# Kernel optimization log

Hardware: AMD Instinct MI355X
Metric: run time of the kernel (lower is better)

## Reference

```python
import jax, jax.numpy as jnp
import numpy as np

N, K, D = 16384, 8192, 256  # flattened tokens, codebook size, token dim


def setup_inputs() -> dict:
    key = jax.random.key(0)
    k1, k2 = jax.random.split(key)
    inputs_flatten = jax.random.normal(k1, (N, D), dtype=jnp.float32)
    embed = jax.random.normal(k2, (K, D), dtype=jnp.float32)
    return {"inputs_flatten": inputs_flatten, "embed": embed}


def reference(inputs_flatten, embed):
    x_sq = jnp.sum(inputs_flatten ** 2, axis=1, keepdims=True)          # [N, 1]
    e_sq = jnp.sum(embed ** 2, axis=1)                                  # [K]
    distances = x_sq + e_sq - 2.0 * (inputs_flatten @ embed.T)          # [N, K]
    encoding_indices = jnp.argmin(distances, axis=1)                    # [N]
    # encodings @ embed with one-hot encodings == gather rows of embed
    quantize = embed[encoding_indices]                                  # [N, D]
    # straight-through estimator
    quantize = jax.lax.stop_gradient(quantize - inputs_flatten) + inputs_flatten
    return quantize, encoding_indices[:, None]
```

## Files before the change

### kernel.cpp

```cpp
#include <hip/hip_runtime.h>
#include <float.h>
#include <limits.h>
#include <stdint.h>

constexpr int N = 16384;
constexpr int K = 8192;
constexpr int D = 256;

typedef _Float16 half8_t __attribute__((ext_vector_type(8)));
typedef float float4_t __attribute__((ext_vector_type(4)));

__global__ void vq_rowsq(const float* __restrict__ A, float* __restrict__ out) {
    int row = blockIdx.x;
    int lane = threadIdx.x;
    float4 v = ((const float4*)(A + (size_t)row * D))[lane];
    float s = v.x * v.x + v.y * v.y + v.z * v.z + v.w * v.w;
    #pragma unroll
    for (int o = 32; o > 0; o >>= 1) s += __shfl_down(s, o);
    if (lane == 0) out[row] = s;
}


__global__ void vq_prep(const float* __restrict__ X, const float* __restrict__ E,
                        _Float16* __restrict__ Xh, _Float16* __restrict__ Eh,
                        float* __restrict__ esq) {
    int c = blockIdx.x * 256 + threadIdx.x;
    const int XCH = N * 32;
    if (c < XCH) {
        int row = c >> 5, q8 = c & 31;
        int ds = q8 >> 2, q = q8 & 3;
        int rt = row >> 7, lr = row & 127;
        int slot = ((lr >> 4) << 6) + (q << 4) + (lr & 15);
        size_t dst = ((size_t)rt * 4096 + ds * 512 + slot) * 8;
        const float4* s4 = (const float4*)(X + (size_t)row * D + q8 * 8);
        float4 v0 = s4[0], v1 = s4[1];
        float x[8] = {v0.x, v0.y, v0.z, v0.w, v1.x, v1.y, v1.z, v1.w};
        half8_t hh;
        #pragma unroll
        for (int i = 0; i < 8; i++) hh[i] = (_Float16)x[i];
        *(half8_t*)(Xh + dst) = hh;
    } else {
        int cc = c - XCH;
        int code = cc >> 5, q8 = cc & 31;
        int ds = q8 >> 2, q = q8 & 3;
        int ct = code >> 7, lc = code & 127;
        int slot = ((lc >> 4) << 6) + (q << 4) + (lc & 15);
        size_t dst = ((size_t)(ct * 8 + ds) * 512 + slot) * 8;
        const float4* s4 = (const float4*)(E + (size_t)code * D + q8 * 8);
        float4 v0 = s4[0], v1 = s4[1];
        float x[8] = {v0.x, v0.y, v0.z, v0.w, v1.x, v1.y, v1.z, v1.w};
        half8_t hh;
        float sq = 0.f;
        #pragma unroll
        for (int i = 0; i < 8; i++) {
            hh[i] = (_Float16)x[i];
            sq += x[i] * x[i];
        }
        *(half8_t*)(Eh + dst) = hh;
        #pragma unroll
        for (int o = 16; o > 0; o >>= 1) sq += __shfl_xor(sq, o);
        if ((threadIdx.x & 31) == 0) esq[code] = sq;
    }
}

__device__ __forceinline__ void ldg_lds16(const _Float16* g, _Float16* l) {
    __builtin_amdgcn_global_load_lds(
        (const __attribute__((address_space(1))) unsigned int*)g,
        (__attribute__((address_space(3))) unsigned int*)l, 16, 0, 0);
}

constexpr int CS = 8;
constexpr int KT = (K / 128) / CS;
constexpr int NSTEP = KT * 8;

__global__ __launch_bounds__(256, 2) void vq_mfma(
    const _Float16* __restrict__ Xh, const _Float16* __restrict__ Eh,
    const float* __restrict__ esq, float4* __restrict__ pcand) {
    __shared__ _Float16 lds[32768];

    const int t = threadIdx.x, w = t >> 6, lane = t & 63;
    const int rt = blockIdx.x;
    const int cs = blockIdx.y;
    const int c15 = lane & 15, quad = lane >> 4;

    float best[16];
    int bidx[16];
    #pragma unroll
    for (int i = 0; i < 16; i++) { best[i] = FLT_MAX; bidx[i] = 0; }

    {
        const _Float16* src = Xh + ((size_t)rt * 4096 + w * 1024) * 8;
        _Float16* dst = lds + (size_t)(w * 1024) * 8;
        #pragma unroll
        for (int i = 0; i < 16; i++)
            ldg_lds16(src + (size_t)(i * 64 + lane) * 8, dst + i * 512);
    }

    const half8_t* C = (const half8_t*)lds;
    const int abase = (w >> 1) * 256 + lane;
    const half8_t* Bf = (const half8_t*)Eh;
    const int bbase = (w & 1) * 256 + lane;

    float4_t acc[4][4];
    #pragma unroll
    for (int mt = 0; mt < 4; mt++)
        #pragma unroll
        for (int nt = 0; nt < 4; nt++) acc[mt][nt] = {0.f, 0.f, 0.f, 0.f};

    half8_t Breg[2][4];
    auto loadB = [&](int s, int par) {
        const size_t rbase = (size_t)(cs * KT * 8 + s) * 512 + bbase;
        #pragma unroll
        for (int nt = 0; nt < 4; nt++) Breg[par][nt] = Bf[rbase + nt * 64];
    };

    loadB(0, 0);
    __syncthreads();

    #pragma unroll 2
    for (int s = 0; s < NSTEP; s++) {
        if (s + 1 < NSTEP) loadB(s + 1, (s + 1) & 1);

        const int ds = s & 7;
        half8_t A[4];
        #pragma unroll
        for (int mt = 0; mt < 4; mt++) A[mt] = C[ds * 512 + abase + mt * 64];

        #pragma unroll
        for (int mt = 0; mt < 4; mt++)
            #pragma unroll
            for (int nt = 0; nt < 4; nt++)
                acc[mt][nt] = __builtin_amdgcn_mfma_f32_16x16x32_f16(
                    A[mt], Breg[s & 1][nt], acc[mt][nt], 0, 0, 0);

        if ((s & 7) == 7) {
            const int code0 = (cs * KT + (s >> 3)) * 128 + (w & 1) * 64;
            #pragma unroll
            for (int nt = 0; nt < 4; nt++) {
                const int code = code0 + nt * 16 + c15;
                const float eq = esq[code];
                #pragma unroll
                for (int mt = 0; mt < 4; mt++)
                    #pragma unroll
                    for (int rg = 0; rg < 4; rg++) {
                        float sc = fmaf(-2.f, acc[mt][nt][rg], eq);
                        int sl = mt * 4 + rg;
                        if (sc < best[sl]) { best[sl] = sc; bidx[sl] = code; }
                    }
            }
            #pragma unroll
            for (int mt = 0; mt < 4; mt++)
                #pragma unroll
                for (int nt = 0; nt < 4; nt++) acc[mt][nt] = {0.f, 0.f, 0.f, 0.f};
        }
    }

    __syncthreads();
    float* smin = (float*)lds;
    int* sidx = (int*)lds + 4096;
    const int cont = (w & 1) * 16 + c15;
    #pragma unroll
    for (int sl = 0; sl < 16; sl++) {
        int row = (w >> 1) * 64 + (sl >> 2) * 16 + quad * 4 + (sl & 3);
        smin[cont * 128 + row] = best[sl];
        sidx[cont * 128 + row] = bidx[sl];
    }
    __syncthreads();
    if (t < 128) {
        float m1 = FLT_MAX, m2 = FLT_MAX;
        int i1 = 0, i2 = 0;
        for (int c = 0; c < 32; c++) {
            float v = smin[c * 128 + t];
            int id = sidx[c * 128 + t];
            if (v < m1 || (v == m1 && id < i1)) {
                m2 = m1; i2 = i1; m1 = v; i1 = id;
            } else if (v < m2 || (v == m2 && id < i2)) {
                m2 = v; i2 = id;
            }
        }
        uint32_t pk = ((uint32_t)i1 << 13) | (uint32_t)(i2 & 8191);
        float4 out;
        out.x = m1; out.y = m2; out.z = __int_as_float((int)pk); out.w = 0.f;
        pcand[(size_t)(rt * 128 + t) * CS + cs] = out;
    }
}

__device__ __forceinline__ float wave_sum(float v) {
    #pragma unroll
    for (int o = 1; o < 64; o <<= 1) v += __shfl_xor(v, o);
    return v;
}

__global__ void vq_rescore(const float* __restrict__ X, const float* __restrict__ E,
                           const float4* __restrict__ pcand, float* __restrict__ out_q,
                           float* __restrict__ out_idx) {
    constexpr float EB = 0.4f;
    int row = blockIdx.x * 4 + (threadIdx.x >> 6);
    int lane = threadIdx.x & 63;

    int cand[2 * CS];
    float csc[2 * CS];
    float gm1 = FLT_MAX, gm2 = FLT_MAX;
    int gi1 = INT_MAX;
    #pragma unroll
    for (int s = 0; s < CS; s++) {
        float4 p = pcand[(size_t)row * CS + s];
        uint32_t pk = (uint32_t)__float_as_int(p.z);
        int i1 = (int)(pk >> 13), i2 = (int)(pk & 8191);
        cand[2 * s] = i1;
        csc[2 * s] = p.x;
        cand[2 * s + 1] = i2;
        csc[2 * s + 1] = p.y;
        if (p.x < gm1 || (p.x == gm1 && i1 < gi1)) {
            gm2 = gm1; gm1 = p.x; gi1 = i1;
        } else if (p.x < gm2) gm2 = p.x;
        if (p.y < gm2) gm2 = p.y;
    }

    int besti = gi1;
    if (gm2 - gm1 <= EB) {
        float4 xv = ((const float4*)(X + (size_t)row * D))[lane];
        float xs = wave_sum(xv.x * xv.x + xv.y * xv.y + xv.z * xv.z + xv.w * xv.w);
        float bestv = FLT_MAX;
        besti = INT_MAX;
        for (int c = 0; c < 2 * CS; c++) {
            if (csc[c] > gm1 + EB) continue;
            int idx = cand[c];
            float4 e = ((const float4*)(E + (size_t)idx * D))[lane];
            float dp = wave_sum(xv.x * e.x + xv.y * e.y + xv.z * e.z + xv.w * e.w);
            float eq = wave_sum(e.x * e.x + e.y * e.y + e.z * e.z + e.w * e.w);
            float sc = (xs + eq) - 2.f * dp;
            if (sc < bestv || (sc == bestv && idx < besti)) { bestv = sc; besti = idx; }
        }
    }
    if (lane == 0) out_idx[row] = (float)besti;
    float4 bv = ((const float4*)(E + (size_t)besti * D))[lane];
    ((float4*)(out_q + (size_t)row * D))[lane] = bv;
}

constexpr int BM = 128, BN = 128, DK = 32, KSPLIT = 8;
constexpr int KCHUNK = K / KSPLIT;
constexpr int LDX = BM + 4, LDE = BN + 4;

__global__ __launch_bounds__(256) void vq_main(
    const float* __restrict__ X, const float* __restrict__ E,
    const float* __restrict__ xsq, const float* __restrict__ esq,
    float* __restrict__ pmin, int* __restrict__ pidx) {
    __shared__ float sx[DK * LDX];
    __shared__ float se[DK * LDE];
    const int t = threadIdx.x;
    const int row0 = blockIdx.x * BM;
    const int kbeg = blockIdx.y * KCHUNK;
    const int lane = t & 63, wave = t >> 6;
    const int lm = lane >> 3, ln = lane & 7;
    const int mf = (wave >> 1) * 64 + lm * 8;
    const int nf = (wave & 1) * 64 + ln * 8;
    float xs[8];
    #pragma unroll
    for (int i = 0; i < 8; i++) xs[i] = xsq[row0 + mf + i];
    float rmin[8];
    int ridx[8];
    #pragma unroll
    for (int i = 0; i < 8; i++) { rmin[i] = FLT_MAX; ridx[i] = 0; }
    const int sm = t >> 3;
    const int sd = (t & 7) * 4;
    for (int kt = kbeg; kt < kbeg + KCHUNK; kt += BN) {
        float acc[8][8];
        #pragma unroll
        for (int i = 0; i < 8; i++)
            #pragma unroll
            for (int j = 0; j < 8; j++) acc[i][j] = 0.0f;
        for (int d0 = 0; d0 < D; d0 += DK) {
            __syncthreads();
            #pragma unroll
            for (int r = 0; r < 4; r++) {
                int row = sm + 32 * r;
                float4 v = *(const float4*)(X + (size_t)(row0 + row) * D + d0 + sd);
                sx[(sd + 0) * LDX + row] = v.x;
                sx[(sd + 1) * LDX + row] = v.y;
                sx[(sd + 2) * LDX + row] = v.z;
                sx[(sd + 3) * LDX + row] = v.w;
                float4 ww = *(const float4*)(E + (size_t)(kt + row) * D + d0 + sd);
                se[(sd + 0) * LDE + row] = ww.x;
                se[(sd + 1) * LDE + row] = ww.y;
                se[(sd + 2) * LDE + row] = ww.z;
                se[(sd + 3) * LDE + row] = ww.w;
            }
            __syncthreads();
            #pragma unroll
            for (int d = 0; d < DK; d++) {
                float4 a0 = *(const float4*)(sx + d * LDX + mf);
                float4 a1 = *(const float4*)(sx + d * LDX + mf + 4);
                float4 b0 = *(const float4*)(se + d * LDE + nf);
                float4 b1 = *(const float4*)(se + d * LDE + nf + 4);
                float a[8] = {a0.x, a0.y, a0.z, a0.w, a1.x, a1.y, a1.z, a1.w};
                float b[8] = {b0.x, b0.y, b0.z, b0.w, b1.x, b1.y, b1.z, b1.w};
                #pragma unroll
                for (int i = 0; i < 8; i++)
                    #pragma unroll
                    for (int j = 0; j < 8; j++) acc[i][j] += a[i] * b[j];
            }
        }
        float es[8];
        #pragma unroll
        for (int j = 0; j < 8; j++) es[j] = esq[kt + nf + j];
        #pragma unroll
        for (int i = 0; i < 8; i++)
            #pragma unroll
            for (int j = 0; j < 8; j++) {
                float s = (xs[i] + es[j]) - 2.0f * acc[i][j];
                if (s < rmin[i]) { rmin[i] = s; ridx[i] = kt + nf + j; }
            }
    }
    __syncthreads();
    float* redm = sx;
    int* redi = (int*)se;
    const int c = (wave & 1) * 8 + ln;
    #pragma unroll
    for (int i = 0; i < 8; i++) {
        int r = (wave >> 1) * 64 + lm * 8 + i;
        redm[r * 16 + c] = rmin[i];
        redi[r * 16 + c] = ridx[i];
    }
    __syncthreads();
    if (t < BM) {
        float bst = redm[t * 16];
        int bi = redi[t * 16];
        #pragma unroll
        for (int c2 = 1; c2 < 16; c2++) {
            float v = redm[t * 16 + c2];
            int id = redi[t * 16 + c2];
            if (v < bst || (v == bst && id < bi)) { bst = v; bi = id; }
        }
        pmin[(size_t)(row0 + t) * KSPLIT + blockIdx.y] = bst;
        pidx[(size_t)(row0 + t) * KSPLIT + blockIdx.y] = bi;
    }
}

__global__ void vq_final(const float* __restrict__ E, const float* __restrict__ pmin,
                         const int* __restrict__ pidx, float* __restrict__ out_q,
                         float* __restrict__ out_idx) {
    int row = blockIdx.x;
    int lane = threadIdx.x;
    float bst = pmin[(size_t)row * KSPLIT];
    int bi = pidx[(size_t)row * KSPLIT];
    #pragma unroll
    for (int s = 1; s < KSPLIT; s++) {
        float v = pmin[(size_t)row * KSPLIT + s];
        int id = pidx[(size_t)row * KSPLIT + s];
        if (v < bst || (v == bst && id < bi)) { bst = v; bi = id; }
    }
    if (lane == 0) out_idx[row] = (float)bi;
    float4 v = ((const float4*)(E + (size_t)bi * D))[lane];
    ((float4*)(out_q + (size_t)row * D))[lane] = v;
}

extern "C" void kernel_launch(void* const* d_in, const int* in_sizes, int n_in,
                              void* d_out, int out_size, void* d_ws, size_t ws_size,
                              hipStream_t stream) {
    const float* X = (const float*)d_in[0];
    const float* E = (const float*)d_in[1];
    float* out_q = (float*)d_out;
    float* out_idx = (float*)d_out + (size_t)N * D;

    const size_t need = (size_t)12 * 1024 * 1024 + 32768 + (size_t)N * CS * 16;
    if (ws_size >= need) {
        _Float16* Xh = (_Float16*)d_ws;
        _Float16* Eh = Xh + (size_t)N * D;
        float* esq = (float*)(Eh + (size_t)K * D);
        float4* pcand = (float4*)(esq + K);

        vq_prep<<<(N + K) * 32 / 256, 256, 0, stream>>>(X, E, Xh, Eh, esq);
        dim3 grid(N / 128, CS);
        vq_mfma<<<grid, 256, 0, stream>>>(Xh, Eh, esq, pcand);
        vq_rescore<<<N / 4, 256, 0, stream>>>(X, E, pcand, out_q, out_idx);
    } else {
        float* esq = (float*)d_ws;
        float* xsq = esq + K;
        float* pmin = xsq + N;
        int* pidx = (int*)(pmin + (size_t)N * KSPLIT);
        vq_rowsq<<<K, 64, 0, stream>>>(E, esq);
        vq_rowsq<<<N, 64, 0, stream>>>(X, xsq);
        dim3 grid(N / BM, KSPLIT);
        vq_main<<<grid, 256, 0, stream>>>(X, E, xsq, esq, pmin, pidx);
        vq_final<<<N, 64, 0, stream>>>(E, pmin, pidx, out_q, out_idx);
    }
}
```

Baseline: 160.3 us.

## Swap operand roles: keep X in registers, stream codebook tiles through double-buffered LDS

The MFMA kernel is restructured so each 512-thread block owns 512 rows. X fragments are read directly from global memory and codebook tiles of 128 codes are staged into double-buffered LDS with async global-to-LDS loads. Each wave now computes a 64x128 tile with 32 accumulators, and the esq loads are hoisted per code tile. The grid shrinks to 32x8 = 256 blocks with larger LDS use. This raises register pressure and may limit occupancy, and it re-reads X from global memory on every code tile.

Measured after the change: 149.9 us. -6.4%, faster.

```diff
diff --git a/kernel.cpp b/kernel.cpp
--- a/kernel.cpp
+++ b/kernel.cpp
@@ -71,15 +71,16 @@
 
 constexpr int CS = 8;
 constexpr int KT = (K / 128) / CS;
-constexpr int NSTEP = KT * 8;
-
-__global__ __launch_bounds__(256, 2) void vq_mfma(
+constexpr int RT = 32;
+constexpr int ROWS = N / RT;
+
+__global__ __launch_bounds__(512, 2) void vq_mfma(
     const _Float16* __restrict__ Xh, const _Float16* __restrict__ Eh,
     const float* __restrict__ esq, float4* __restrict__ pcand) {
-    __shared__ _Float16 lds[32768];
+    __shared__ _Float16 lds[65536];
 
     const int t = threadIdx.x, w = t >> 6, lane = t & 63;
-    const int rt = blockIdx.x;
+    const int rs = blockIdx.x;
     const int cs = blockIdx.y;
     const int c15 = lane & 15, quad = lane >> 4;
 
@@ -88,90 +89,91 @@
     #pragma unroll
     for (int i = 0; i < 16; i++) { best[i] = FLT_MAX; bidx[i] = 0; }
 
-    {
-        const _Float16* src = Xh + ((size_t)rt * 4096 + w * 1024) * 8;
-        _Float16* dst = lds + (size_t)(w * 1024) * 8;
-        #pragma unroll
-        for (int i = 0; i < 16; i++)
-            ldg_lds16(src + (size_t)(i * 64 + lane) * 8, dst + i * 512);
-    }
-
-    const half8_t* C = (const half8_t*)lds;
-    const int abase = (w >> 1) * 256 + lane;
-    const half8_t* Bf = (const half8_t*)Eh;
-    const int bbase = (w & 1) * 256 + lane;
-
-    float4_t acc[4][4];
+    const half8_t* Xg = (const half8_t*)Xh +
+        ((size_t)(rs * 4 + (w >> 1)) * 4096 + (w & 1) * 256 + lane);
+
+    const half8_t* Eg = (const half8_t*)Eh + (size_t)(cs * KT) * 4096;
+
+    auto stage = [&](int ct, int b) {
+        const half8_t* src = Eg + ((size_t)ct * 4096 + w * 512 + lane);
+        _Float16* dst = lds + ((size_t)b * 4096 + w * 512) * 8;
+        #pragma unroll
+        for (int i = 0; i < 8; i++)
+            ldg_lds16((const _Float16*)(src + i * 64), dst + i * 512);
+    };
+
+    float4_t acc[4][8];
     #pragma unroll
     for (int mt = 0; mt < 4; mt++)
         #pragma unroll
-        for (int nt = 0; nt < 4; nt++) acc[mt][nt] = {0.f, 0.f, 0.f, 0.f};
-
-    half8_t Breg[2][4];
-    auto loadB = [&](int s, int par) {
-        const size_t rbase = (size_t)(cs * KT * 8 + s) * 512 + bbase;
-        #pragma unroll
-        for (int nt = 0; nt < 4; nt++) Breg[par][nt] = Bf[rbase + nt * 64];
-    };
-
-    loadB(0, 0);
+        for (int nt = 0; nt < 8; nt++) acc[mt][nt] = {0.f, 0.f, 0.f, 0.f};
+
+    float eq[8];
+
+    stage(0, 0);
     __syncthreads();
 
-    #pragma unroll 2
-    for (int s = 0; s < NSTEP; s++) {
-        if (s + 1 < NSTEP) loadB(s + 1, (s + 1) & 1);
-
-        const int ds = s & 7;
-        half8_t A[4];
-        #pragma unroll
-        for (int mt = 0; mt < 4; mt++) A[mt] = C[ds * 512 + abase + mt * 64];
-
-        #pragma unroll
-        for (int mt = 0; mt < 4; mt++)
-            #pragma unroll
-            for (int nt = 0; nt < 4; nt++)
-                acc[mt][nt] = __builtin_amdgcn_mfma_f32_16x16x32_f16(
-                    A[mt], Breg[s & 1][nt], acc[mt][nt], 0, 0, 0);
-
-        if ((s & 7) == 7) {
-            const int code0 = (cs * KT + (s >> 3)) * 128 + (w & 1) * 64;
-            #pragma unroll
-            for (int nt = 0; nt < 4; nt++) {
-                const int code = code0 + nt * 16 + c15;
-                const float eq = esq[code];
-                #pragma unroll
-                for (int mt = 0; mt < 4; mt++)
-                    #pragma unroll
-                    for (int rg = 0; rg < 4; rg++) {
-                        float sc = fmaf(-2.f, acc[mt][nt][rg], eq);
-                        int sl = mt * 4 + rg;
-                        if (sc < best[sl]) { best[sl] = sc; bidx[sl] = code; }
-                    }
-            }
+    for (int ct = 0; ct < KT; ct++) {
+        if (ct + 1 < KT) stage(ct + 1, (ct + 1) & 1);
+
+        const int code0 = (cs * KT + ct) * 128;
+        #pragma unroll
+        for (int nt = 0; nt < 8; nt++) eq[nt] = esq[code0 + nt * 16 + c15];
+
+        const half8_t* Cc = (const half8_t*)lds + (size_t)(ct & 1) * 4096;
+
+        #pragma unroll 2
+        for (int ds = 0; ds < 8; ds++) {
+            half8_t Xf[4];
+            #pragma unroll
+            for (int mt = 0; mt < 4; mt++) Xf[mt] = Xg[ds * 512 + mt * 64];
+            half8_t Ef[8];
+            #pragma unroll
+            for (int nt = 0; nt < 8; nt++) Ef[nt] = Cc[ds * 512 + nt * 64 + lane];
+
             #pragma unroll
             for (int mt = 0; mt < 4; mt++)
                 #pragma unroll
-                for (int nt = 0; nt < 4; nt++) acc[mt][nt] = {0.f, 0.f, 0.f, 0.f};
-        }
-    }
-
+                for (int nt = 0; nt < 8; nt++)
+                    acc[mt][nt] = __builtin_amdgcn_mfma_f32_16x16x32_f16(
+                        Xf[mt], Ef[nt], acc[mt][nt], 0, 0, 0);
+        }
+
+        #pragma unroll
+        for (int nt = 0; nt < 8; nt++) {
+            const int code = code0 + nt * 16 + c15;
+            #pragma unroll
+            for (int mt = 0; mt < 4; mt++)
+                #pragma unroll
+                for (int rg = 0; rg < 4; rg++) {
+                    float sc = fmaf(-2.f, acc[mt][nt][rg], eq[nt]);
+                    int sl = mt * 4 + rg;
+                    if (sc < best[sl]) { best[sl] = sc; bidx[sl] = code; }
+                }
+        }
+        #pragma unroll
+        for (int mt = 0; mt < 4; mt++)
+            #pragma unroll
+            for (int nt = 0; nt < 8; nt++) acc[mt][nt] = {0.f, 0.f, 0.f, 0.f};
+
+        __syncthreads();
+    }
+
+    float* smin = (float*)lds;
+    int* sidx = (int*)lds + 8192;
+    #pragma unroll
+    for (int sl = 0; sl < 16; sl++) {
+        int row = w * 64 + (sl >> 2) * 16 + quad * 4 + (sl & 3);
+        smin[c15 * 512 + row] = best[sl];
+        sidx[c15 * 512 + row] = bidx[sl];
+    }
     __syncthreads();
-    float* smin = (float*)lds;
-    int* sidx = (int*)lds + 4096;
-    const int cont = (w & 1) * 16 + c15;
-    #pragma unroll
-    for (int sl = 0; sl < 16; sl++) {
-        int row = (w >> 1) * 64 + (sl >> 2) * 16 + quad * 4 + (sl & 3);
-        smin[cont * 128 + row] = best[sl];
-        sidx[cont * 128 + row] = bidx[sl];
-    }
-    __syncthreads();
-    if (t < 128) {
+    {
         float m1 = FLT_MAX, m2 = FLT_MAX;
         int i1 = 0, i2 = 0;
-        for (int c = 0; c < 32; c++) {
-            float v = smin[c * 128 + t];
-            int id = sidx[c * 128 + t];
+        for (int c = 0; c < 16; c++) {
+            float v = smin[c * 512 + t];
+            int id = sidx[c * 512 + t];
             if (v < m1 || (v == m1 && id < i1)) {
                 m2 = m1; i2 = i1; m1 = v; i1 = id;
             } else if (v < m2 || (v == m2 && id < i2)) {
@@ -181,7 +183,7 @@
         uint32_t pk = ((uint32_t)i1 << 13) | (uint32_t)(i2 & 8191);
         float4 out;
         out.x = m1; out.y = m2; out.z = __int_as_float((int)pk); out.w = 0.f;
-        pcand[(size_t)(rt * 128 + t) * CS + cs] = out;
+        pcand[(size_t)(rs * 512 + t) * CS + cs] = out;
     }
 }
 
@@ -371,8 +373,8 @@
         float4* pcand = (float4*)(esq + K);
 
         vq_prep<<<(N + K) * 32 / 256, 256, 0, stream>>>(X, E, Xh, Eh, esq);
-        dim3 grid(N / 128, CS);
-        vq_mfma<<<grid, 256, 0, stream>>>(Xh, Eh, esq, pcand);
+        dim3 grid(RT, CS);
+        vq_mfma<<<grid, 512, 0, stream>>>(Xh, Eh, esq, pcand);
         vq_rescore<<<N / 4, 256, 0, stream>>>(X, E, pcand, out_q, out_idx);
     } else {
         float* esq = (float*)d_ws;
```
